# Performance work log

Measured on AMD Instinct MI355X. Metric: run time of the kernel, lower is better.

The kernel has to match this reference:

```python
import jax, jax.numpy as jnp
import numpy as np

N_NODES = 100000
N_EDGES = 1600000
NODE_DIM = 128
HIDDEN = 128
OUT_DIM = 128
N_GRAPHS = 64
LN_EPS = 1e-5


def setup_inputs() -> dict:
    key = jax.random.key(0)
    ks = jax.random.split(key, 14)

    def lin(k, fan_in, fan_out):
        bound = 1.0 / np.sqrt(fan_in)
        kw, kb = jax.random.split(k)
        W = jax.random.uniform(kw, (fan_in, fan_out), jnp.float32, -bound, bound)
        b = jax.random.uniform(kb, (fan_out,), jnp.float32, -bound, bound)
        return W, b

    node_features = jax.random.normal(ks[0], (N_NODES, NODE_DIM), jnp.float32)
    edge_index = jax.random.randint(ks[1], (2, N_EDGES), 0, N_NODES, jnp.int32)
    batch = jnp.sort(jax.random.randint(ks[2], (N_NODES,), 0, N_GRAPHS, jnp.int32))

    W1, b1 = lin(ks[3], NODE_DIM, HIDDEN)
    W2, b2 = lin(ks[4], HIDDEN, HIDDEN)
    W3, b3 = lin(ks[5], HIDDEN, OUT_DIM)
    Wm1, bm1 = lin(ks[6], OUT_DIM, HIDDEN)
    Wm2, bm2 = lin(ks[7], HIDDEN, OUT_DIM)
    ln_g = jnp.ones((OUT_DIM,), jnp.float32)
    ln_b = jnp.zeros((OUT_DIM,), jnp.float32)

    return dict(node_features=node_features, edge_index=edge_index, batch=batch,
                W1=W1, b1=b1, W2=W2, b2=b2, W3=W3, b3=b3,
                Wm1=Wm1, bm1=bm1, Wm2=Wm2, bm2=bm2, ln_g=ln_g, ln_b=ln_b)


def _gcn_precompute(edge_index, n_nodes):
    # Add self-loops; symmetric degree normalization (PyG GCNConv semantics).
    loops = jnp.arange(n_nodes, dtype=edge_index.dtype)
    src = jnp.concatenate([edge_index[0], loops])
    dst = jnp.concatenate([edge_index[1], loops])
    deg = jax.ops.segment_sum(jnp.ones_like(dst, jnp.float32), dst, num_segments=n_nodes)
    dinv = jax.lax.rsqrt(deg)  # deg >= 1 thanks to self-loops
    norm = dinv[src] * dinv[dst]  # [E + N]
    return src, dst, norm


def _gcn_layer(x, W, b, src, dst, norm, n_nodes):
    xw = x @ W                              # [N, F_out]
    msg = norm[:, None] * xw[src]           # [E+N, F_out] gather
    agg = jax.ops.segment_sum(msg, dst, num_segments=n_nodes)  # scatter-add
    return agg + b


def reference(node_features, edge_index, batch,
              W1, b1, W2, b2, W3, b3, Wm1, bm1, Wm2, bm2, ln_g, ln_b):
    n_nodes = node_features.shape[0]
    src, dst, norm = _gcn_precompute(edge_index, n_nodes)

    x = jax.nn.relu(_gcn_layer(node_features, W1, b1, src, dst, norm, n_nodes))
    x = jax.nn.relu(_gcn_layer(x, W2, b2, src, dst, norm, n_nodes))
    x = _gcn_layer(x, W3, b3, src, dst, norm, n_nodes)  # no relu on last layer

    # global mean pool per graph
    sums = jax.ops.segment_sum(x, batch, num_segments=N_GRAPHS)
    cnts = jax.ops.segment_sum(jnp.ones((n_nodes,), x.dtype), batch, num_segments=N_GRAPHS)
    g = sums / jnp.maximum(cnts, 1.0)[:, None]  # [G, OUT_DIM]

    # global reasoner MLP + LayerNorm
    h = jax.nn.relu(g @ Wm1 + bm1)
    y = h @ Wm2 + bm2
    mu = jnp.mean(y, axis=-1, keepdims=True)
    var = jnp.var(y, axis=-1, keepdims=True)
    y = (y - mu) * jax.lax.rsqrt(var + LN_EPS) * ln_g + ln_b
    return y
```

## Files before the change

kernel.cpp:

```cpp
#include <hip/hip_runtime.h>

#define FDIM 128
#define LN_EPS 1e-5f
#define NBKT_SHIFT 8
#define BKT_NODES 256
#define MAXBKT 512
#define CAP_SHIFT 13
#define BKT_CAP 8192

typedef short bf16x8 __attribute__((ext_vector_type(8)));
typedef float f32x4 __attribute__((ext_vector_type(4)));
typedef float f32x2 __attribute__((ext_vector_type(2)));
typedef ushort u16x8 __attribute__((ext_vector_type(8)));
typedef unsigned long long u64;
typedef long long i64;

static __device__ __forceinline__ ushort f2bf(float f) {
    union { float f; unsigned u; } v; v.f = f;
    unsigned r = v.u + 0x7FFFu + ((v.u >> 16) & 1u);
    return (ushort)(r >> 16);
}
static __device__ __forceinline__ float bf2f(ushort h) {
    union { unsigned u; float f; } v; v.u = ((unsigned)h) << 16;
    return v.f;
}
static __device__ __forceinline__ unsigned char f2fp8(float f) {
    return (unsigned char)__builtin_amdgcn_cvt_pk_fp8_f32(f, f, 0u, false);
}
static __device__ __forceinline__ float fp8tof(unsigned char b) {
    f32x2 p = __builtin_amdgcn_cvt_pk_f32_fp8((unsigned)b, false);
    return p[0];
}
static __device__ __forceinline__ void fp8x8_add(uint2 w, f32x2* acc) {
    acc[0] += __builtin_amdgcn_cvt_pk_f32_fp8(w.x, false);
    acc[1] += __builtin_amdgcn_cvt_pk_f32_fp8(w.x, true);
    acc[2] += __builtin_amdgcn_cvt_pk_f32_fp8(w.y, false);
    acc[3] += __builtin_amdgcn_cvt_pk_f32_fp8(w.y, true);
}


__launch_bounds__(256)
__global__ void k_bkt_scatter(const int* __restrict__ src, const int* __restrict__ dst,
                              int* __restrict__ bcur, unsigned* __restrict__ bktA,
                              int E, int nbkt) {
    __shared__ int h[2][MAXBKT], lbase[2][MAXBKT], lcur[2][MAXBKT];
    const int t = threadIdx.x;
    const int half = t >> 7;
    for (int i = t; i < 2 * MAXBKT; i += 256) ((int*)h)[i] = 0;
    __syncthreads();
    const int E4 = E >> 2;
    const int4* s4p = (const int4*)src;
    const int4* d4p = (const int4*)dst;
    int4 sv[4], dv[4]; bool ok[4];
#pragma unroll
    for (int r = 0; r < 4; r++) {
        int i4 = blockIdx.x * 1024 + r * 256 + t;
        ok[r] = (i4 < E4);
        if (ok[r]) {
            sv[r] = s4p[i4]; dv[r] = d4p[i4];
            atomicAdd(&h[half][dv[r].x >> NBKT_SHIFT], 1);
            atomicAdd(&h[half][dv[r].y >> NBKT_SHIFT], 1);
            atomicAdd(&h[half][dv[r].z >> NBKT_SHIFT], 1);
            atomicAdd(&h[half][dv[r].w >> NBKT_SHIFT], 1);
        }
    }
    __syncthreads();
    for (int i = t; i < 2 * nbkt; i += 256) {
        const int hh = (i >= nbkt) ? 1 : 0;
        const int b = hh ? (i - nbkt) : i;
        const int c = h[hh][b];
        lbase[hh][b] = c ? ((b << CAP_SHIFT) + atomicAdd(&bcur[b], c)) : 0;
        lcur[hh][b] = 0;
    }
    __syncthreads();
#pragma unroll
    for (int r = 0; r < 4; r++) {
        if (!ok[r]) continue;
        int ss[4] = {sv[r].x, sv[r].y, sv[r].z, sv[r].w};
        int dd[4] = {dv[r].x, dv[r].y, dv[r].z, dv[r].w};
#pragma unroll
        for (int j = 0; j < 4; j++) {
            int b = dd[j] >> NBKT_SHIFT;
            int p = atomicAdd(&lcur[half][b], 1);
            bktA[(size_t)lbase[half][b] + p] =
                ((unsigned)ss[j] << NBKT_SHIFT) | (unsigned)(dd[j] & (BKT_NODES - 1));
        }
    }
}


__launch_bounds__(512)
__global__ void k_build(const unsigned* __restrict__ bktA, const int* __restrict__ bcur,
                        int2* __restrict__ rowinfo, float* __restrict__ dinv,
                        int* __restrict__ csr_src, int N) {
    __shared__ int sorted[BKT_CAP];
    __shared__ int cnt[BKT_NODES];
    __shared__ int cur[BKT_NODES];
    __shared__ int wpart[4], wbase[4];
    const int t = threadIdx.x;
    const int b = blockIdx.x;
    const int nb = b << NBKT_SHIFT;
    if (t < BKT_NODES) cnt[t] = 0;
    __syncthreads();
    const int beg = b << CAP_SHIFT;
    const int tot = bcur[b];
    for (int i = t; i < tot; i += 512)
        atomicAdd(&cnt[bktA[beg + i] & (BKT_NODES - 1)], 1);
    __syncthreads();
    const int lane = t & 63, wv = t >> 6;
    int my = 0, x = 0;
    if (t < BKT_NODES) {
        my = cnt[t];
        x = my;
#pragma unroll
        for (int off = 1; off < 64; off <<= 1) {
            int y = __shfl_up(x, off, 64);
            if (lane >= off) x += y;
        }
        if (lane == 63) wpart[wv] = x;
    }
    __syncthreads();
    if (t == 0) {
        int s = 0;
        for (int w = 0; w < 4; w++) { int tmp = wpart[w]; wbase[w] = s; s += tmp; }
    }
    __syncthreads();
    if (t < BKT_NODES) {
        const int incl = x + wbase[wv];
        const int rbeg = incl - my;
        cur[t] = rbeg;
        const int n = nb + t;
        if (n < N) {
            rowinfo[n] = make_int2(beg + rbeg, my);
            dinv[n] = rsqrtf((float)(my + 1));
        }
    }
    __syncthreads();
    for (int i = t; i < tot; i += 512) {
        unsigned pr = bktA[beg + i];
        int d = pr & (BKT_NODES - 1);
        int p = atomicAdd(&cur[d], 1);
        sorted[p] = (int)(pr >> NBKT_SHIFT);
    }
    __syncthreads();
    for (int i = t; i < tot; i += 512)
        csr_src[beg + i] = sorted[i];
}


__global__ void k_prep_w(const float* __restrict__ Wa, const float* __restrict__ Wb,
                         const float* __restrict__ Wc, ushort* __restrict__ Wt_b,
                         unsigned char* __restrict__ Wt8, float* __restrict__ gsums,
                         int* __restrict__ bcur) {
    int idx = blockIdx.x * 256 + threadIdx.x;
    int layer = idx >> 14;
    int r = idx & 16383;
    int nn = r >> 7, kk = r & 127;
    if (layer == 0) {
        Wt_b[r] = f2bf(Wa[kk * 128 + nn]);
    } else {
        const float* W = (layer == 1) ? Wb : Wc;
        Wt8[(size_t)(layer - 1) * 16384 + r] = f2fp8(W[kk * 128 + nn]);
    }
    if (idx < 8192) gsums[idx] = 0.f;
    if (idx < MAXBKT) bcur[idx] = 0;
}


__launch_bounds__(256)
__global__ void k_gemm_f32(const float* __restrict__ X, const ushort* __restrict__ Wt,
                           const float* __restrict__ dinv, unsigned char* __restrict__ C,
                           int N) {
    __shared__ __align__(16) ushort As[128][136];
    __shared__ ushort Ws[128][136];
    const int t = threadIdx.x;
    const int row0 = blockIdx.x * 128;

#pragma unroll
    for (int i = 0; i < 8; i++) {
        int c = t + i * 256;
        int r = c >> 4, c8 = (c & 15) * 8;
        *(bf16x8*)&Ws[r][c8] = *(const bf16x8*)&Wt[r * 128 + c8];
    }
#pragma unroll
    for (int i = 0; i < 8; i++) {
        int c = t + i * 256;
        int r = c >> 4, c8 = (c & 15) * 8;
        int row = row0 + r;
        bf16x8 pk = {0, 0, 0, 0, 0, 0, 0, 0};
        if (row < N) {
            const float* sp = X + (size_t)row * FDIM + c8;
            float4 u0 = *(const float4*)(sp);
            float4 u1 = *(const float4*)(sp + 4);
            pk[0] = (short)f2bf(u0.x); pk[1] = (short)f2bf(u0.y);
            pk[2] = (short)f2bf(u0.z); pk[3] = (short)f2bf(u0.w);
            pk[4] = (short)f2bf(u1.x); pk[5] = (short)f2bf(u1.y);
            pk[6] = (short)f2bf(u1.z); pk[7] = (short)f2bf(u1.w);
        }
        *(bf16x8*)&As[r][c8] = pk;
    }
    __syncthreads();

    const int w = t >> 6, l = t & 63;
    const int m = l & 15, q = l >> 4;
    const int r0 = w * 32;

    bf16x8 a0[4], a1[4];
#pragma unroll
    for (int ks = 0; ks < 4; ks++) {
        a0[ks] = *(const bf16x8*)&As[r0 + m][ks * 32 + q * 8];
        a1[ks] = *(const bf16x8*)&As[r0 + 16 + m][ks * 32 + q * 8];
    }

    f32x4 acc0[8], acc1[8];
#pragma unroll
    for (int ct = 0; ct < 8; ct++) { acc0[ct] = {0, 0, 0, 0}; acc1[ct] = {0, 0, 0, 0}; }

#pragma unroll
    for (int ct = 0; ct < 8; ct++) {
#pragma unroll
        for (int ks = 0; ks < 4; ks++) {
            bf16x8 b = *(const bf16x8*)&Ws[ct * 16 + m][ks * 32 + q * 8];
            acc0[ct] = __builtin_amdgcn_mfma_f32_16x16x32_bf16(a0[ks], b, acc0[ct], 0, 0, 0);
            acc1[ct] = __builtin_amdgcn_mfma_f32_16x16x32_bf16(a1[ks], b, acc1[ct], 0, 0, 0);
        }
    }

    float dv0[4], dv1[4];
#pragma unroll
    for (int r = 0; r < 4; r++) {
        int row = row0 + r0 + q * 4 + r;
        dv0[r] = (row < N) ? dinv[row] : 0.f;
        dv1[r] = (row + 16 < N) ? dinv[row + 16] : 0.f;
    }

    __syncthreads();
    char* Ab = (char*)&As[0][0];
#pragma unroll
    for (int ct = 0; ct < 8; ct++) {
#pragma unroll
        for (int r = 0; r < 4; r++) {
            int rl = r0 + q * 4 + r;
            Ab[rl * 128 + ct * 16 + m] = (char)f2fp8(acc0[ct][r] * dv0[r]);
            Ab[(rl + 16) * 128 + ct * 16 + m] = (char)f2fp8(acc1[ct][r] * dv1[r]);
        }
    }
    __syncthreads();
    const uint4* As4 = (const uint4*)Ab;
#pragma unroll
    for (int i = 0; i < 4; i++) {
        int c = t + i * 256;
        int row = c >> 3;
        int col = (c & 7) * 16;
        int grow = row0 + row;
        if (grow < N) *(uint4*)&C[(size_t)grow * FDIM + col] = As4[c];
    }
}


__launch_bounds__(256)
__global__ void k_gemm_fp8(const unsigned char* __restrict__ X,
                           const unsigned char* __restrict__ W8,
                           const float* __restrict__ dinv, unsigned char* __restrict__ C,
                           int N) {
    __shared__ __align__(16) unsigned char As[128][144];
    __shared__ __align__(16) unsigned char Ws[128][144];
    const int t = threadIdx.x;
    const int row0 = blockIdx.x * 128;

#pragma unroll
    for (int i = 0; i < 4; i++) {
        int c = t + i * 256;
        int r = c >> 3, col = (c & 7) * 16;
        *(uint4*)&Ws[r][col] = *(const uint4*)&W8[r * 128 + col];
        int row = row0 + r;
        uint4 v = {0, 0, 0, 0};
        if (row < N) v = *(const uint4*)&X[(size_t)row * FDIM + col];
        *(uint4*)&As[r][col] = v;
    }
    __syncthreads();

    const int w = t >> 6, l = t & 63;
    const int m = l & 15, q = l >> 4;
    const int r0 = w * 32;

    i64 a0[4], a1[4];
#pragma unroll
    for (int ks = 0; ks < 4; ks++) {
        a0[ks] = *(const i64*)&As[r0 + m][ks * 32 + q * 8];
        a1[ks] = *(const i64*)&As[r0 + 16 + m][ks * 32 + q * 8];
    }

    f32x4 acc0[8], acc1[8];
#pragma unroll
    for (int ct = 0; ct < 8; ct++) { acc0[ct] = {0, 0, 0, 0}; acc1[ct] = {0, 0, 0, 0}; }

#pragma unroll
    for (int ct = 0; ct < 8; ct++) {
#pragma unroll
        for (int ks = 0; ks < 4; ks++) {
            i64 b = *(const i64*)&Ws[ct * 16 + m][ks * 32 + q * 8];
            acc0[ct] = __builtin_amdgcn_mfma_f32_16x16x32_fp8_fp8(a0[ks], b, acc0[ct], 0, 0, 0);
            acc1[ct] = __builtin_amdgcn_mfma_f32_16x16x32_fp8_fp8(a1[ks], b, acc1[ct], 0, 0, 0);
        }
    }

    float dv0[4], dv1[4];
#pragma unroll
    for (int r = 0; r < 4; r++) {
        int row = row0 + r0 + q * 4 + r;
        dv0[r] = (row < N) ? dinv[row] : 0.f;
        dv1[r] = (row + 16 < N) ? dinv[row + 16] : 0.f;
    }

    __syncthreads();
    char* Ab = (char*)&As[0][0];
#pragma unroll
    for (int ct = 0; ct < 8; ct++) {
#pragma unroll
        for (int r = 0; r < 4; r++) {
            int rl = r0 + q * 4 + r;
            Ab[rl * 128 + ct * 16 + m] = (char)f2fp8(acc0[ct][r] * dv0[r]);
            Ab[(rl + 16) * 128 + ct * 16 + m] = (char)f2fp8(acc1[ct][r] * dv1[r]);
        }
    }
    __syncthreads();
    const uint4* As4 = (const uint4*)Ab;
#pragma unroll
    for (int i = 0; i < 4; i++) {
        int c = t + i * 256;
        int row = c >> 3;
        int col = (c & 7) * 16;
        int grow = row0 + row;
        if (grow < N) *(uint4*)&C[(size_t)grow * FDIM + col] = As4[c];
    }
}


__launch_bounds__(256)
__global__ void k_aggregate(const unsigned char* __restrict__ xs8,
                            const int2* __restrict__ rowinfo,
                            const int* __restrict__ csr_src, const float* __restrict__ dinv,
                            const float* __restrict__ bias, unsigned char* __restrict__ out,
                            const int* __restrict__ batch, float* __restrict__ gsums,
                            int N, int do_relu, int fuse_pool) {
    __shared__ float gsum_s[FDIM];
    __shared__ int gb_s[8];
    const int t = threadIdx.x;
    const int l = t & 63;
    const int node_slot = t >> 5;
    const int n = blockIdx.x * 8 + node_slot;
    const bool active = (n < N);
    const int hl = l & 31;
    const int fl = hl & 15;
    const int grp = hl >> 4;
    const int selbase = l & 32;
    const unsigned foff = (unsigned)fl << 3;

    if (fuse_pool) {
        if (t < FDIM) gsum_s[t] = 0.f;
        if (t < 8) {
            int nn = blockIdx.x * 8 + t;
            gb_s[t] = batch[nn < N ? nn : (N - 1)];
        }
        __syncthreads();
    }

    f32x2 acc[4] = {{0, 0}, {0, 0}, {0, 0}, {0, 0}};
    int2 ri = active ? rowinfo[n] : make_int2(0, 0);
    if (active && grp == 0) {
        uint2 sv = *(const uint2*)(xs8 + (((unsigned)n << 7) | foff));
        fp8x8_add(sv, acc);
    }
    const int beg = ri.x;
    const int deg = ri.y;

    for (int base = 0; base < deg; base += 32) {
        const int m = min(32, deg - base);
        int idx = 0;
        if (hl < m) idx = csr_src[(unsigned)(beg + base + hl)];
        int j = grp;
        if (j < m) {
            int s0 = __shfl(idx, selbase | j, 64);
            uint2 v0 = *(const uint2*)(xs8 + (((unsigned)s0 << 7) | foff));
            int j1 = j + 2;
            if (j1 < m) {
                int s1 = __shfl(idx, selbase | j1, 64);
                uint2 v1 = *(const uint2*)(xs8 + (((unsigned)s1 << 7) | foff));
                int j2 = j1 + 2;
                if (j2 < m) {
                    int s2 = __shfl(idx, selbase | j2, 64);
                    uint2 v2 = *(const uint2*)(xs8 + (((unsigned)s2 << 7) | foff));
                    for (j = j2 + 2; j < m; j += 2) {
                        int s3 = __shfl(idx, selbase | j, 64);
                        uint2 v3 = *(const uint2*)(xs8 + (((unsigned)s3 << 7) | foff));
                        fp8x8_add(v0, acc);
                        v0 = v1; v1 = v2; v2 = v3;
                    }
                    fp8x8_add(v0, acc);
                    fp8x8_add(v1, acc);
                    fp8x8_add(v2, acc);
                } else {
                    fp8x8_add(v0, acc);
                    fp8x8_add(v1, acc);
                }
            } else {
                fp8x8_add(v0, acc);
            }
        }
    }

    float a[8] = {acc[0][0], acc[0][1], acc[1][0], acc[1][1],
                  acc[2][0], acc[2][1], acc[3][0], acc[3][1]};
#pragma unroll
    for (int k = 0; k < 8; k++) a[k] += __shfl_xor(a[k], 16, 64);

    if (active && grp == 0) {
        const float d = dinv[n];
        const float4 b0 = ((const float4*)bias)[fl * 2];
        const float4 b1 = ((const float4*)bias)[fl * 2 + 1];
        const float bb[8] = {b0.x, b0.y, b0.z, b0.w, b1.x, b1.y, b1.z, b1.w};
        float v[8];
#pragma unroll
        for (int k = 0; k < 8; k++) {
            v[k] = d * a[k] + bb[k];
            if (do_relu) v[k] = fmaxf(v[k], 0.f);
        }
        if (!fuse_pool) {
            uint2 o;
            unsigned d0 = __builtin_amdgcn_cvt_pk_fp8_f32(v[0], v[1], 0u, false);
            o.x = __builtin_amdgcn_cvt_pk_fp8_f32(v[2], v[3], d0, true);
            unsigned d1 = __builtin_amdgcn_cvt_pk_fp8_f32(v[4], v[5], 0u, false);
            o.y = __builtin_amdgcn_cvt_pk_fp8_f32(v[6], v[7], d1, true);
            ((uint2*)out)[(size_t)n * 16 + fl] = o;
        } else {
            const bool uni = (gb_s[0] == gb_s[7]);
            if (uni) {
#pragma unroll
                for (int k = 0; k < 8; k++) atomicAdd(&gsum_s[foff + k], v[k]);
            } else {
                const int g = gb_s[node_slot];
#pragma unroll
                for (int k = 0; k < 8; k++) atomicAdd(&gsums[g * FDIM + foff + k], v[k]);
            }
        }
    }
    if (fuse_pool) {
        __syncthreads();
        if (gb_s[0] == gb_s[7]) {
            if (t < FDIM) atomicAdd(&gsums[gb_s[0] * FDIM + t], gsum_s[t]);
        }
    }
}


__launch_bounds__(128)
__global__ void k_final(const float* __restrict__ sums, const int* __restrict__ batch, int N,
                        const float* __restrict__ Wm1, const float* __restrict__ bm1,
                        const float* __restrict__ Wm2, const float* __restrict__ bm2,
                        const float* __restrict__ ln_g, const float* __restrict__ ln_b,
                        float* __restrict__ out) {
    const int g = blockIdx.x;
    const int t = threadIdx.x;

    int lo = 0, hi = N;
    while (lo < hi) { int mid = (lo + hi) >> 1; if (batch[mid] < g) lo = mid + 1; else hi = mid; }
    int lo2 = lo, hi2 = N;
    while (lo2 < hi2) { int mid = (lo2 + hi2) >> 1; if (batch[mid] < g + 1) lo2 = mid + 1; else hi2 = mid; }
    float cnt = (float)(lo2 - lo);

    float gl = sums[g * FDIM + t] / fmaxf(cnt, 1.0f);

    __shared__ float gbuf[FDIM];
    __shared__ float hbuf[FDIM];
    __shared__ float wsum[4];
    gbuf[t] = gl;
    __syncthreads();

    float h = bm1[t];
#pragma unroll 8
    for (int k = 0; k < FDIM; k++) h += gbuf[k] * Wm1[k * FDIM + t];
    h = fmaxf(h, 0.f);
    hbuf[t] = h;
    __syncthreads();

    float y = bm2[t];
#pragma unroll 8
    for (int k = 0; k < FDIM; k++) y += hbuf[k] * Wm2[k * FDIM + t];

    float s = y, s2 = y * y;
#pragma unroll
    for (int off = 32; off > 0; off >>= 1) {
        s += __shfl_down(s, off, 64);
        s2 += __shfl_down(s2, off, 64);
    }
    if ((t & 63) == 0) { wsum[t >> 6] = s; wsum[2 + (t >> 6)] = s2; }
    __syncthreads();
    float sum = wsum[0] + wsum[1];
    float sumsq = wsum[2] + wsum[3];
    float mu = sum * (1.0f / FDIM);
    float var = sumsq * (1.0f / FDIM) - mu * mu;
    float r = rsqrtf(var + LN_EPS);
    out[g * FDIM + t] = (y - mu) * r * ln_g[t] + ln_b[t];
}


extern "C" void kernel_launch(void* const* d_in, const int* in_sizes, int n_in,
                              void* d_out, int out_size, void* d_ws, size_t ws_size,
                              hipStream_t stream) {
    const float* x_in  = (const float*)d_in[0];
    const int*   eidx  = (const int*)d_in[1];
    const int*   batch = (const int*)d_in[2];
    const float* W1 = (const float*)d_in[3];
    const float* b1 = (const float*)d_in[4];
    const float* W2 = (const float*)d_in[5];
    const float* b2 = (const float*)d_in[6];
    const float* W3 = (const float*)d_in[7];
    const float* b3 = (const float*)d_in[8];
    const float* Wm1 = (const float*)d_in[9];
    const float* bm1 = (const float*)d_in[10];
    const float* Wm2 = (const float*)d_in[11];
    const float* bm2 = (const float*)d_in[12];
    const float* ln_g = (const float*)d_in[13];
    const float* ln_b = (const float*)d_in[14];
    float* out = (float*)d_out;

    const int N = in_sizes[0] / FDIM;
    const int E = in_sizes[1] / 2;
    const int G = out_size / FDIM;

    const int* src = eidx;
    const int* dst = eidx + E;

    const int nbkt = (N + BKT_NODES - 1) >> NBKT_SHIFT;

    char* p = (char*)d_ws;
    unsigned* bktA = (unsigned*)p;    p += (size_t)nbkt * BKT_CAP * 4;
    unsigned char* B0q = (unsigned char*)p; p += (size_t)N * FDIM;
    unsigned char* B1q = (unsigned char*)p; p += (size_t)N * FDIM;
    int* csr_src = (int*)p;           p += (size_t)nbkt * BKT_CAP * 4;
    int2* rowinfo = (int2*)p;         p += (size_t)N * 8;
    float* dinv = (float*)p;          p += (size_t)N * 4;
    ushort* Wt_b = (ushort*)p;        p += 16384 * 2;
    unsigned char* Wt8 = (unsigned char*)p; p += 2 * 16384;
    float* gsums = (float*)p;         p += (size_t)G * FDIM * 4;
    int* bcur = (int*)p;              p += MAXBKT * 4;

    const int TPB = 256;
    dim3 blk(TPB);
    dim3 gAgg((N + 7) / 8);
    dim3 gTile((N + 127) / 128);
    const int nEb = (E + 4095) / 4096;

    k_prep_w<<<dim3(192), blk, 0, stream>>>(W1, W2, W3, Wt_b, Wt8, gsums, bcur);
    k_bkt_scatter<<<dim3(nEb), blk, 0, stream>>>(src, dst, bcur, bktA, E, nbkt);
    k_build<<<dim3(nbkt), dim3(512), 0, stream>>>(bktA, bcur, rowinfo, dinv, csr_src, N);

    k_gemm_f32<<<gTile, blk, 0, stream>>>(x_in, Wt_b, dinv, B0q, N);
    k_aggregate<<<gAgg, blk, 0, stream>>>(B0q, rowinfo, csr_src, dinv, b1, B1q,
                                          batch, gsums, N, 1, 0);

    k_gemm_fp8<<<gTile, blk, 0, stream>>>(B1q, Wt8, dinv, B0q, N);
    k_aggregate<<<gAgg, blk, 0, stream>>>(B0q, rowinfo, csr_src, dinv, b2, B1q,
                                          batch, gsums, N, 1, 0);

    k_gemm_fp8<<<gTile, blk, 0, stream>>>(B1q, Wt8 + 16384, dinv, B0q, N);
    k_aggregate<<<gAgg, blk, 0, stream>>>(B0q, rowinfo, csr_src, dinv, b3, B1q,
                                          batch, gsums, N, 0, 1);

    k_final<<<dim3(G), dim3(FDIM), 0, stream>>>(gsums, batch, N, Wm1, bm1, Wm2, bm2,
                                                ln_g, ln_b, out);
}
```

Baseline: 388.5 us.

## Use direct global-to-LDS loads in fp8 GEMM and one wave per node in aggregation

The fp8 GEMM now loads its A and W tiles with global_load_lds straight into unpadded LDS, replacing the register-staged copies. The aggregation kernel gives each node a full 64-lane wave with four edge groups instead of a 32-lane half-wave with two, fetches 64 neighbour indices per batch, and adds a second cross-lane reduction step. The aim is more memory-level parallelism per node and less load overhead in the GEMM. In exchange, dropping the LDS row padding may cause bank conflicts on the MFMA operand reads, many lanes sit idle for low-degree nodes, and the aggregation launches twice as many blocks. The GEMM also no longer checks row < N when loading, so the last tile reads past the end of X.

```diff
diff --git a/kernel.cpp b/kernel.cpp
--- a/kernel.cpp
+++ b/kernel.cpp
@@ -36,6 +36,12 @@
     acc[1] += __builtin_amdgcn_cvt_pk_f32_fp8(w.x, true);
     acc[2] += __builtin_amdgcn_cvt_pk_f32_fp8(w.y, false);
     acc[3] += __builtin_amdgcn_cvt_pk_f32_fp8(w.y, true);
+}
+
+typedef __attribute__((address_space(3))) unsigned char lds_uchar;
+typedef const __attribute__((address_space(1))) unsigned char glob_uchar;
+static __device__ __forceinline__ void gload16(const unsigned char* g, unsigned char* l) {
+    __builtin_amdgcn_global_load_lds((glob_uchar*)g, (lds_uchar*)l, 16, 0, 0);
 }
 
 
@@ -263,32 +269,33 @@
                            const unsigned char* __restrict__ W8,
                            const float* __restrict__ dinv, unsigned char* __restrict__ C,
                            int N) {
-    __shared__ __align__(16) unsigned char As[128][144];
-    __shared__ __align__(16) unsigned char Ws[128][144];
+    __shared__ __align__(16) unsigned char As[128 * 128];
+    __shared__ __align__(16) unsigned char Ws[128 * 128];
     const int t = threadIdx.x;
+    const int w = t >> 6, l = t & 63;
     const int row0 = blockIdx.x * 128;
 
-#pragma unroll
-    for (int i = 0; i < 4; i++) {
-        int c = t + i * 256;
-        int r = c >> 3, col = (c & 7) * 16;
-        *(uint4*)&Ws[r][col] = *(const uint4*)&W8[r * 128 + col];
-        int row = row0 + r;
-        uint4 v = {0, 0, 0, 0};
-        if (row < N) v = *(const uint4*)&X[(size_t)row * FDIM + col];
-        *(uint4*)&As[r][col] = v;
-    }
-    __syncthreads();
-
-    const int w = t >> 6, l = t & 63;
+    {
+        const int lrow = (l >> 3);
+        const int lcol = (l & 7) * 16;
+        const unsigned char* gx = X + (size_t)(row0 + w * 32 + lrow) * FDIM + lcol;
+        const unsigned char* gw = W8 + (size_t)(w * 32 + lrow) * FDIM + lcol;
+#pragma unroll
+        for (int i = 0; i < 4; i++) {
+            gload16(gx + (size_t)i * 8 * FDIM, &As[(w * 32 + i * 8) * FDIM]);
+            gload16(gw + (size_t)i * 8 * FDIM, &Ws[(w * 32 + i * 8) * FDIM]);
+        }
+    }
+    __syncthreads();
+
     const int m = l & 15, q = l >> 4;
     const int r0 = w * 32;
 
     i64 a0[4], a1[4];
 #pragma unroll
     for (int ks = 0; ks < 4; ks++) {
-        a0[ks] = *(const i64*)&As[r0 + m][ks * 32 + q * 8];
-        a1[ks] = *(const i64*)&As[r0 + 16 + m][ks * 32 + q * 8];
+        a0[ks] = *(const i64*)&As[(r0 + m) * FDIM + ks * 32 + q * 8];
+        a1[ks] = *(const i64*)&As[(r0 + 16 + m) * FDIM + ks * 32 + q * 8];
     }
 
     f32x4 acc0[8], acc1[8];
@@ -299,7 +306,7 @@
     for (int ct = 0; ct < 8; ct++) {
 #pragma unroll
         for (int ks = 0; ks < 4; ks++) {
-            i64 b = *(const i64*)&Ws[ct * 16 + m][ks * 32 + q * 8];
+            i64 b = *(const i64*)&Ws[(ct * 16 + m) * FDIM + ks * 32 + q * 8];
             acc0[ct] = __builtin_amdgcn_mfma_f32_16x16x32_fp8_fp8(a0[ks], b, acc0[ct], 0, 0, 0);
             acc1[ct] = __builtin_amdgcn_mfma_f32_16x16x32_fp8_fp8(a1[ks], b, acc1[ct], 0, 0, 0);
         }
@@ -314,7 +321,7 @@
     }
 
     __syncthreads();
-    char* Ab = (char*)&As[0][0];
+    char* Ab = (char*)&As[0];
 #pragma unroll
     for (int ct = 0; ct < 8; ct++) {
 #pragma unroll
@@ -345,65 +352,54 @@
                             const int* __restrict__ batch, float* __restrict__ gsums,
                             int N, int do_relu, int fuse_pool) {
     __shared__ float gsum_s[FDIM];
-    __shared__ int gb_s[8];
+    __shared__ int gb_s[4];
     const int t = threadIdx.x;
+    const int n = (blockIdx.x << 2) + (t >> 6);
+    const bool active = (n < N);
     const int l = t & 63;
-    const int node_slot = t >> 5;
-    const int n = blockIdx.x * 8 + node_slot;
-    const bool active = (n < N);
-    const int hl = l & 31;
-    const int fl = hl & 15;
-    const int grp = hl >> 4;
-    const int selbase = l & 32;
+    const int fl = l & 15;
+    const int grp = l >> 4;
     const unsigned foff = (unsigned)fl << 3;
 
     if (fuse_pool) {
         if (t < FDIM) gsum_s[t] = 0.f;
-        if (t < 8) {
-            int nn = blockIdx.x * 8 + t;
+        if (t < 4) {
+            int nn = (blockIdx.x << 2) + t;
             gb_s[t] = batch[nn < N ? nn : (N - 1)];
         }
         __syncthreads();
     }
 
     f32x2 acc[4] = {{0, 0}, {0, 0}, {0, 0}, {0, 0}};
-    int2 ri = active ? rowinfo[n] : make_int2(0, 0);
     if (active && grp == 0) {
         uint2 sv = *(const uint2*)(xs8 + (((unsigned)n << 7) | foff));
         fp8x8_add(sv, acc);
     }
+
+    const int2 ri = active ? rowinfo[n] : make_int2(0, 0);
     const int beg = ri.x;
     const int deg = ri.y;
 
-    for (int base = 0; base < deg; base += 32) {
-        const int m = min(32, deg - base);
+    for (int base = 0; base < deg; base += 64) {
+        const int m = min(64, deg - base);
         int idx = 0;
-        if (hl < m) idx = csr_src[(unsigned)(beg + base + hl)];
+        if (l < m) idx = csr_src[(unsigned)(beg + base + l)];
         int j = grp;
         if (j < m) {
-            int s0 = __shfl(idx, selbase | j, 64);
+            int s0 = __shfl(idx, j, 64);
             uint2 v0 = *(const uint2*)(xs8 + (((unsigned)s0 << 7) | foff));
-            int j1 = j + 2;
-            if (j1 < m) {
-                int s1 = __shfl(idx, selbase | j1, 64);
+            int j2 = j + 4;
+            if (j2 < m) {
+                int s1 = __shfl(idx, j2, 64);
                 uint2 v1 = *(const uint2*)(xs8 + (((unsigned)s1 << 7) | foff));
-                int j2 = j1 + 2;
-                if (j2 < m) {
-                    int s2 = __shfl(idx, selbase | j2, 64);
+                for (j = j2 + 4; j < m; j += 4) {
+                    int s2 = __shfl(idx, j, 64);
                     uint2 v2 = *(const uint2*)(xs8 + (((unsigned)s2 << 7) | foff));
-                    for (j = j2 + 2; j < m; j += 2) {
-                        int s3 = __shfl(idx, selbase | j, 64);
-                        uint2 v3 = *(const uint2*)(xs8 + (((unsigned)s3 << 7) | foff));
-                        fp8x8_add(v0, acc);
-                        v0 = v1; v1 = v2; v2 = v3;
-                    }
                     fp8x8_add(v0, acc);
-                    fp8x8_add(v1, acc);
-                    fp8x8_add(v2, acc);
-                } else {
-                    fp8x8_add(v0, acc);
-                    fp8x8_add(v1, acc);
+                    v0 = v1; v1 = v2;
                 }
+                fp8x8_add(v0, acc);
+                fp8x8_add(v1, acc);
             } else {
                 fp8x8_add(v0, acc);
             }
@@ -413,7 +409,10 @@
     float a[8] = {acc[0][0], acc[0][1], acc[1][0], acc[1][1],
                   acc[2][0], acc[2][1], acc[3][0], acc[3][1]};
 #pragma unroll
-    for (int k = 0; k < 8; k++) a[k] += __shfl_xor(a[k], 16, 64);
+    for (int k = 0; k < 8; k++) {
+        a[k] += __shfl_xor(a[k], 16, 64);
+        a[k] += __shfl_xor(a[k], 32, 64);
+    }
 
     if (active && grp == 0) {
         const float d = dinv[n];
@@ -434,12 +433,12 @@
             o.y = __builtin_amdgcn_cvt_pk_fp8_f32(v[6], v[7], d1, true);
             ((uint2*)out)[(size_t)n * 16 + fl] = o;
         } else {
-            const bool uni = (gb_s[0] == gb_s[7]);
+            const bool uni = (gb_s[0] == gb_s[3]);
             if (uni) {
 #pragma unroll
                 for (int k = 0; k < 8; k++) atomicAdd(&gsum_s[foff + k], v[k]);
             } else {
-                const int g = gb_s[node_slot];
+                const int g = gb_s[t >> 6];
 #pragma unroll
                 for (int k = 0; k < 8; k++) atomicAdd(&gsums[g * FDIM + foff + k], v[k]);
             }
@@ -447,9 +446,7 @@
     }
     if (fuse_pool) {
         __syncthreads();
-        if (gb_s[0] == gb_s[7]) {
-            if (t < FDIM) atomicAdd(&gsums[gb_s[0] * FDIM + t], gsum_s[t]);
-        }
+        if (gb_s[0] == gb_s[3] && t < FDIM) atomicAdd(&gsums[gb_s[0] * FDIM + t], gsum_s[t]);
     }
 }
 
@@ -548,7 +545,7 @@
 
     const int TPB = 256;
     dim3 blk(TPB);
-    dim3 gAgg((N + 7) / 8);
+    dim3 gAgg((N + 3) / 4);
     dim3 gTile((N + 127) / 128);
     const int nEb = (E + 4095) / 4096;
 
```

Result: slower. 455.2 us (+17.2%).
